# Kernel tuning notes

Measured on AMD Instinct MI355X. Metric: run time of the kernel, lower is better.

## Reference

```python
import jax, jax.numpy as jnp
import numpy as np

B, L, D, H, E, K = 4, 2048, 1024, 2048, 8, 2


def _mlp(x, w1, b1, w2, b2):
    # Mlp: Linear -> GELU(tanh) -> Linear (dropout disabled / eval mode)
    h = jax.nn.gelu(x @ w1 + b1, approximate=True)
    return h @ w2 + b2


def setup_inputs() -> dict:
    key = jax.random.key(0)
    ks = jax.random.split(key, 16)
    s = 0.02
    inp = {
        "x": jax.random.normal(ks[0], (B, L, D), dtype=jnp.float32),
        "task_ids": jax.random.randint(ks[1], (B,), 0, 9),
        # gate: Linear(D,H) -> GELU -> Linear(H,E)  (zero-init in source; randomized here for a meaningful routing test)
        "gw1": jax.random.normal(ks[2], (D, H), dtype=jnp.float32) * s,
        "gb1": jnp.zeros((H,), dtype=jnp.float32),
        "gw2": jax.random.normal(ks[3], (H, E), dtype=jnp.float32) * s,
        "gb2": jnp.zeros((E,), dtype=jnp.float32),
        # routed experts, stacked [E, ...]
        "We1": jax.random.normal(ks[4], (E, D, H), dtype=jnp.float32) * s,
        "be1": jnp.zeros((E, H), dtype=jnp.float32),
        "We2": jax.random.normal(ks[5], (E, H, D), dtype=jnp.float32) * s,
        "be2": jnp.zeros((E, D), dtype=jnp.float32),
        # shared expert
        "Ws1": jax.random.normal(ks[6], (D, H), dtype=jnp.float32) * s,
        "bs1": jnp.zeros((H,), dtype=jnp.float32),
        "Ws2": jax.random.normal(ks[7], (H, D), dtype=jnp.float32) * s,
        "bs2": jnp.zeros((D,), dtype=jnp.float32),
    }
    return inp


def reference(x, task_ids, gw1, gb1, gw2, gb2, We1, be1, We2, be2, Ws1, bs1, Ws2, bs2):
    bsz, length, d = x.shape
    T = bsz * length
    xf = x.reshape(T, d)

    # ---- top-k gating (single gate: moe_multiple_gate=False) ----
    logits = jax.nn.gelu(xf @ gw1 + gb1, approximate=False) @ gw2 + gb2  # [T, E]
    scores = jax.nn.softmax(logits, axis=-1)
    topk_w, topk_idx = jax.lax.top_k(scores, K)  # [T, K]
    # dense gate matrix: scatter top-k weights back (matches compute_gating's gates)
    rows = jnp.arange(T)[:, None]
    gates = jnp.zeros_like(scores).at[rows, topk_idx].set(topk_w)  # [T, E]

    # ---- shared expert (always applied) ----
    out = _mlp(xf, Ws1, bs1, Ws2, bs2)

    # ---- routed experts: dense-equivalent of sort/dispatch/scatter-combine ----
    # y += sum_e gates[:, e] * expert_e(x); loop over small fixed E to bound memory
    for e in range(E):
        out = out + gates[:, e:e + 1] * _mlp(xf, We1[e], be1[e], We2[e], be2[e])

    return out.reshape(bsz, length, d)
```

## Files before the change

### kernel.cpp

```cpp
#include <hip/hip_runtime.h>
#include <hip/hip_bf16.h>


using bf16 = __hip_bfloat16;
typedef __attribute__((ext_vector_type(8))) short short8;
typedef __attribute__((ext_vector_type(4))) float float4v;

#define T_TOK 8192
#define DDIM  1024
#define HDIM  2048
#define NEXP  8

__device__ __forceinline__ float bf2f(short s) {
  unsigned u = ((unsigned)(unsigned short)s) << 16;
  return __builtin_bit_cast(float, u);
}
__device__ __forceinline__ unsigned short f2bf(float f) {
  unsigned u = __builtin_bit_cast(unsigned, f);
  unsigned r = (u + 0x7fffu + ((u >> 16) & 1u)) >> 16;
  return (unsigned short)r;
}
__device__ __forceinline__ float gelu_erf_f(float x) {
  return 0.5f * x * (1.0f + erff(x * 0.70710678118654752f));
}
__device__ __forceinline__ float gelu_tanh_f(float x) {
  float t = tanhf(0.7978845608028654f * (x + 0.044715f * x * x * x));
  return 0.5f * x * (1.0f + t);
}
__device__ __forceinline__ void gld_lds16(const bf16* g, bf16* l) {
  __builtin_amdgcn_global_load_lds(
      (const __attribute__((address_space(1))) void*)g,
      (__attribute__((address_space(3))) void*)l, 16, 0, 0);
}

__global__ __launch_bounds__(256) void cast_split_x(
    const float* __restrict__ x, bf16* __restrict__ xh, bf16* __restrict__ xl)
{
  long i = ((long)blockIdx.x * 256 + threadIdx.x) * 4;
  float4v v = *(const float4v*)(x + i);
  short4 h, l;
  short* hp = (short*)&h; short* lp = (short*)&l;
  #pragma unroll
  for (int j = 0; j < 4; ++j) {
    unsigned short hb = f2bf(v[j]);
    hp[j] = (short)hb;
    lp[j] = (short)f2bf(v[j] - bf2f((short)hb));
  }
  *(short4*)((short*)xh + i) = h;
  *(short4*)((short*)xl + i) = l;
}

template<bool SPLIT>
__global__ __launch_bounds__(256) void transpose_cast(
    const float* __restrict__ in, bf16* __restrict__ out,
    bf16* __restrict__ outl, int R, int C)
{
  __shared__ float tile[32][33];
  long b = blockIdx.z;
  const float* ip = in + b * (long)R * C;
  short* op = (short*)out + b * (long)R * C;
  short* opl = SPLIT ? (short*)outl + b * (long)R * C : nullptr;
  int c0 = blockIdx.x * 32, r0 = blockIdx.y * 32;
  int tx = threadIdx.x & 31, ty = threadIdx.x >> 5;
  #pragma unroll
  for (int i = ty; i < 32; i += 8)
    tile[i][tx] = ip[(long)(r0 + i) * C + c0 + tx];
  __syncthreads();
  #pragma unroll
  for (int i = ty; i < 32; i += 8) {
    float v = tile[tx][i];
    unsigned short hb = f2bf(v);
    op[(long)(c0 + i) * R + r0 + tx] = (short)hb;
    if (SPLIT)
      opl[(long)(c0 + i) * R + r0 + tx] = (short)f2bf(v - bf2f((short)hb));
  }
}

template<int ACT, typename OutT, int GATHER, bool WEIGHTED, bool SPLIT, bool COMBINE>
__global__ __launch_bounds__(256) void gemm_bt(
    const bf16* __restrict__ A, const bf16* __restrict__ Bt,
    const bf16* __restrict__ Al, const bf16* __restrict__ Btl,
    const float* __restrict__ bias, OutT* __restrict__ Cmat,
    int M, int N, int Kd, int ldA,
    long strideB, long strideBias,
    const int* __restrict__ perm, const int* __restrict__ counts,
    const float* __restrict__ wslot, const bf16* __restrict__ RoutC)
{
  __shared__ __align__(16) bf16 lA[128 * 32];
  __shared__ __align__(16) bf16 lB[128 * 32];
  __shared__ int permT[128];

  const int tid = threadIdx.x;
  const int tile_n = blockIdx.x, tile_m = blockIdx.y, z = blockIdx.z;

  int Meff = M;
  if (GATHER) {
    const int* perm_z = perm + (long)z * T_TOK;
    Meff = counts[z];
    if (tile_m * 128 >= Meff) return;
    if (tid < 128) {
      int i = tile_m * 128 + tid;
      permT[tid] = perm_z[i < Meff ? i : (Meff - 1)];
    }
    __syncthreads();
  }
  const float* biasz = bias + (long)z * strideBias;

  const int i0 = tid >> 2;
  const int kc = (((tid & 3) ^ ((tid >> 2) & 3))) * 8;
  long rowA0, rowA1;
  if (GATHER) {
    int p0 = permT[i0], p1 = permT[i0 + 64];
    rowA0 = (GATHER == 1) ? (p0 >> 1) : p0;
    rowA1 = (GATHER == 1) ? (p1 >> 1) : p1;
  } else {
    rowA0 = (long)tile_m * 128 + i0;
    rowA1 = rowA0 + 64;
  }
  bf16* lA0 = &lA[tid * 8];
  bf16* lA1 = &lA[(tid + 256) * 8];
  bf16* lB0 = &lB[tid * 8];
  bf16* lB1 = &lB[(tid + 256) * 8];

  const int lane = tid & 63;
  const int wave = tid >> 6;
  const int wm = (wave & 1) * 64;
  const int wn = (wave >> 1) * 64;
  const int fr = lane & 15;
  const int sw = (((lane >> 4) ^ (lane & 3))) * 8;

  float4v acc[4][4];
  #pragma unroll
  for (int i = 0; i < 4; ++i)
    #pragma unroll
    for (int j = 0; j < 4; ++j) acc[i][j] = {0.f, 0.f, 0.f, 0.f};

  #pragma unroll 1
  for (int ps = 0; ps < (SPLIT ? 3 : 1); ++ps) {
    const bf16* Ap = (SPLIT && ps == 2) ? Al : A;
    const bf16* Bp = (SPLIT && ps == 1) ? Btl : Bt;
    const bf16* aBase0 = Ap + rowA0 * ldA + kc;
    const bf16* aBase1 = Ap + rowA1 * ldA + kc;
    const bf16* bBase0 = Bp + (long)z * strideB
                       + ((long)tile_n * 128 + i0) * Kd + kc;
    const bf16* bBase1 = bBase0 + (long)64 * Kd;

    for (int k0 = 0; k0 < Kd; k0 += 32) {
      gld_lds16(aBase0 + k0, lA0);
      gld_lds16(aBase1 + k0, lA1);
      gld_lds16(bBase0 + k0, lB0);
      gld_lds16(bBase1 + k0, lB1);
      __syncthreads();

      short8 af[4], bfr[4];
      #pragma unroll
      for (int mi = 0; mi < 4; ++mi)
        af[mi] = *(const short8*)&lA[(wm + mi * 16 + fr) * 32 + sw];
      #pragma unroll
      for (int ni = 0; ni < 4; ++ni)
        bfr[ni] = *(const short8*)&lB[(wn + ni * 16 + fr) * 32 + sw];
      #pragma unroll
      for (int mi = 0; mi < 4; ++mi)
        #pragma unroll
        for (int ni = 0; ni < 4; ++ni)
          acc[mi][ni] = __builtin_amdgcn_mfma_f32_16x16x32_bf16(
              af[mi], bfr[ni], acc[mi][ni], 0, 0, 0);
      __syncthreads();
    }
  }

  const int rq = ((lane >> 4)) * 4;
  #pragma unroll
  for (int mi = 0; mi < 4; ++mi) {
    #pragma unroll
    for (int r = 0; r < 4; ++r) {
      int irow = wm + mi * 16 + rq + r;
      int gi = tile_m * 128 + irow;
      long crow;
      bool valid = true;
      float w = 1.f;
      if (GATHER) {
        valid = gi < Meff;
        int p = permT[irow];
        crow = p;
        if (WEIGHTED) w = valid ? wslot[p] : 0.f;
      } else {
        crow = gi;
      }
      if (valid) {
        #pragma unroll
        for (int ni = 0; ni < 4; ++ni) {
          int gcol = tile_n * 128 + wn + ni * 16 + fr;
          float v = acc[mi][ni][r] + biasz[gcol];
          if (ACT == 1) v = gelu_erf_f(v);
          else if (ACT == 2) v = gelu_tanh_f(v);
          if (WEIGHTED) v *= w;
          if (COMBINE) {
            const short* rs = (const short*)RoutC;
            v += bf2f(rs[(2 * crow) * DDIM + gcol])
               + bf2f(rs[(2 * crow + 1) * DDIM + gcol]);
          }
          long cidx = crow * (long)N + gcol;
          if (sizeof(OutT) == 4) ((float*)Cmat)[cidx] = v;
          else ((unsigned short*)Cmat)[cidx] = f2bf(v);
        }
      }
    }
  }
}

__global__ __launch_bounds__(256) void logits_kernel(
    const float* __restrict__ G1, const float* __restrict__ gw2,
    const float* __restrict__ gb2, int* __restrict__ tidx,
    float* __restrict__ wslot)
{
  int wv = threadIdx.x >> 6, lane = threadIdx.x & 63;
  int t = blockIdx.x * 4 + wv;
  const float* grow = G1 + (long)t * HDIM;
  float acc[NEXP];
  #pragma unroll
  for (int e = 0; e < NEXP; ++e) acc[e] = 0.f;
  for (int j = 0; j < HDIM / 64; ++j) {
    int h = j * 64 + lane;
    float g = grow[h];
    float4v w0 = *(const float4v*)&gw2[h * NEXP];
    float4v w1 = *(const float4v*)&gw2[h * NEXP + 4];
    #pragma unroll
    for (int e = 0; e < 4; ++e) {
      acc[e]     += g * w0[e];
      acc[e + 4] += g * w1[e];
    }
  }
  #pragma unroll
  for (int off = 32; off >= 1; off >>= 1)
    #pragma unroll
    for (int e = 0; e < NEXP; ++e) acc[e] += __shfl_xor(acc[e], off);

  if (lane == 0) {
    float lg[NEXP];
    #pragma unroll
    for (int e = 0; e < NEXP; ++e) lg[e] = acc[e] + gb2[e];
    int i1 = 0;
    for (int e = 1; e < NEXP; ++e) if (lg[e] > lg[i1]) i1 = e;
    int i2 = (i1 == 0) ? 1 : 0;
    for (int e = 0; e < NEXP; ++e) {
      if (e == i1) continue;
      if (lg[e] > lg[i2]) i2 = e;
    }
    float m = lg[i1], s = 0.f;
    #pragma unroll
    for (int e = 0; e < NEXP; ++e) s += expf(lg[e] - m);
    float inv = 1.f / s;
    tidx[2 * t]     = i1;
    tidx[2 * t + 1] = i2;
    wslot[2 * t]     = expf(lg[i1] - m) * inv;
    wslot[2 * t + 1] = expf(lg[i2] - m) * inv;
  }
}

__global__ __launch_bounds__(256) void dispatch_kernel(
    const int* __restrict__ tidx, int* __restrict__ counts,
    int* __restrict__ perm)
{
  int t = blockIdx.x * 256 + threadIdx.x;
  int lane = threadIdx.x & 63;
  #pragma unroll
  for (int k = 0; k < 2; ++k) {
    int e = tidx[2 * t + k];
    #pragma unroll
    for (int ex = 0; ex < NEXP; ++ex) {
      unsigned long long m = __ballot(e == ex);
      if (m) {
        int leader = __ffsll((unsigned long long)m) - 1;
        int base = 0;
        if (lane == leader) base = atomicAdd(&counts[ex], __popcll(m));
        base = __shfl(base, leader);
        if (e == ex) {
          int pos = base + __popcll(m & ((1ULL << lane) - 1ULL));
          perm[ex * T_TOK + pos] = 2 * t + k;
        }
      }
    }
  }
}

extern "C" void kernel_launch(void* const* d_in, const int* in_sizes, int n_in,
                              void* d_out, int out_size, void* d_ws, size_t ws_size,
                              hipStream_t stream)
{
  const float* x   = (const float*)d_in[0];
  const float* gw1 = (const float*)d_in[2];
  const float* gb1 = (const float*)d_in[3];
  const float* gw2 = (const float*)d_in[4];
  const float* gb2 = (const float*)d_in[5];
  const float* We1 = (const float*)d_in[6];
  const float* be1 = (const float*)d_in[7];
  const float* We2 = (const float*)d_in[8];
  const float* be2 = (const float*)d_in[9];
  const float* Ws1 = (const float*)d_in[10];
  const float* bs1 = (const float*)d_in[11];
  const float* Ws2 = (const float*)d_in[12];
  const float* bs2 = (const float*)d_in[13];
  float* out = (float*)d_out;

  char* ws = (char*)d_ws;
  bf16*  xb     = (bf16*)(ws + 0);
  bf16*  We1t   = (bf16*)(ws + 16777216);
  bf16*  Rout   = (bf16*)(ws + 16777216);
  bf16*  We2t   = (bf16*)(ws + 50331648);
  bf16*  Ws1t   = (bf16*)(ws + 83886080);
  bf16*  Ws2t   = (bf16*)(ws + 88080384);
  int*   counts = (int*)(ws + 92274688);
  float* wslot  = (float*)(ws + 92275712);
  int*   perm   = (int*)(ws + 92341248);
  bf16*  xl     = (bf16*)(ws + 92603392);
  bf16*  gw1h   = (bf16*)(ws + 109380608);
  bf16*  gw1l   = (bf16*)(ws + 113574912);
  int*   tidx   = (int*)(ws + 113574912);
  float* G1     = (float*)(ws + 117769216);
  bf16*  Hrt    = (bf16*)(ws + 117769216);
  bf16*  S1     = (bf16*)(ws + 117769216);

  hipMemsetAsync(counts, 0, NEXP * sizeof(int), stream);

  dim3 blk(256);
  cast_split_x<<<dim3((T_TOK * DDIM) / 1024), blk, 0, stream>>>(x, xb, xl);
  transpose_cast<true ><<<dim3(HDIM/32, DDIM/32, 1), blk, 0, stream>>>(gw1, gw1h, gw1l, DDIM, HDIM);
  transpose_cast<false><<<dim3(HDIM/32, DDIM/32, 1), blk, 0, stream>>>(Ws1, Ws1t, nullptr, DDIM, HDIM);
  transpose_cast<false><<<dim3(DDIM/32, HDIM/32, 1), blk, 0, stream>>>(Ws2, Ws2t, nullptr, HDIM, DDIM);
  transpose_cast<false><<<dim3(HDIM/32, DDIM/32, NEXP), blk, 0, stream>>>(We1, We1t, nullptr, DDIM, HDIM);
  transpose_cast<false><<<dim3(DDIM/32, HDIM/32, NEXP), blk, 0, stream>>>(We2, We2t, nullptr, HDIM, DDIM);

  gemm_bt<1, float, 0, false, true, false><<<dim3(HDIM/128, T_TOK/128, 1), blk, 0, stream>>>(
      xb, gw1h, xl, gw1l, gb1, G1, T_TOK, HDIM, DDIM, DDIM, 0, 0,
      nullptr, nullptr, nullptr, nullptr);
  logits_kernel<<<dim3(T_TOK / 4), blk, 0, stream>>>(G1, gw2, gb2, tidx, wslot);
  dispatch_kernel<<<dim3(T_TOK / 256), blk, 0, stream>>>(tidx, counts, perm);
  gemm_bt<2, bf16, 1, false, false, false><<<dim3(HDIM/128, T_TOK/128, NEXP), blk, 0, stream>>>(
      xb, We1t, nullptr, nullptr, be1, Hrt, T_TOK, HDIM, DDIM, DDIM,
      (long)HDIM * DDIM, HDIM, perm, counts, nullptr, nullptr);
  gemm_bt<0, bf16, 2, true, false, false><<<dim3(DDIM/128, T_TOK/128, NEXP), blk, 0, stream>>>(
      Hrt, We2t, nullptr, nullptr, be2, Rout, T_TOK, DDIM, HDIM, HDIM,
      (long)DDIM * HDIM, DDIM, perm, counts, wslot, nullptr);
  gemm_bt<2, bf16, 0, false, false, false><<<dim3(HDIM/128, T_TOK/128, 1), blk, 0, stream>>>(
      xb, Ws1t, nullptr, nullptr, bs1, S1, T_TOK, HDIM, DDIM, DDIM, 0, 0,
      nullptr, nullptr, nullptr, nullptr);
  gemm_bt<0, float, 0, false, false, true><<<dim3(DDIM/128, T_TOK/128, 1), blk, 0, stream>>>(
      S1, Ws2t, nullptr, nullptr, bs2, out, T_TOK, DDIM, HDIM, HDIM, 0, 0,
      nullptr, nullptr, nullptr, Rout);
}
```

Baseline: 892.7 us.

## Double K-tile depth and fuse split-precision passes into one K loop

In the non-split path, each K step of the GEMM now loads a 64-wide K slice instead of 32, using a wider XOR swizzle, so each step does twice the MFMA work per pair of barriers. In the split-precision (hi/lo bf16) path, the three separate passes over K are merged into one loop that stages hi and lo tiles of A and B together and issues all three MFMA products per step. The aim is to cut barrier and loop overhead and to avoid reading A and B from global memory three times. In exchange, LDS use doubles, which may reduce occupancy, and register pressure in the fused split path goes up.

```diff
diff --git a/kernel.cpp b/kernel.cpp
--- a/kernel.cpp
+++ b/kernel.cpp
@@ -86,8 +86,8 @@
     const int* __restrict__ perm, const int* __restrict__ counts,
     const float* __restrict__ wslot, const bf16* __restrict__ RoutC)
 {
-  __shared__ __align__(16) bf16 lA[128 * 32];
-  __shared__ __align__(16) bf16 lB[128 * 32];
+  __shared__ __align__(16) bf16 lA[128 * 64];
+  __shared__ __align__(16) bf16 lB[128 * 64];
   __shared__ int permT[128];
 
   const int tid = threadIdx.x;
@@ -106,28 +106,11 @@
   }
   const float* biasz = bias + (long)z * strideBias;
 
-  const int i0 = tid >> 2;
-  const int kc = (((tid & 3) ^ ((tid >> 2) & 3))) * 8;
-  long rowA0, rowA1;
-  if (GATHER) {
-    int p0 = permT[i0], p1 = permT[i0 + 64];
-    rowA0 = (GATHER == 1) ? (p0 >> 1) : p0;
-    rowA1 = (GATHER == 1) ? (p1 >> 1) : p1;
-  } else {
-    rowA0 = (long)tile_m * 128 + i0;
-    rowA1 = rowA0 + 64;
-  }
-  bf16* lA0 = &lA[tid * 8];
-  bf16* lA1 = &lA[(tid + 256) * 8];
-  bf16* lB0 = &lB[tid * 8];
-  bf16* lB1 = &lB[(tid + 256) * 8];
-
   const int lane = tid & 63;
   const int wave = tid >> 6;
   const int wm = (wave & 1) * 64;
   const int wn = (wave >> 1) * 64;
   const int fr = lane & 15;
-  const int sw = (((lane >> 4) ^ (lane & 3))) * 8;
 
   float4v acc[4][4];
   #pragma unroll
@@ -135,36 +118,113 @@
     #pragma unroll
     for (int j = 0; j < 4; ++j) acc[i][j] = {0.f, 0.f, 0.f, 0.f};
 
-  #pragma unroll 1
-  for (int ps = 0; ps < (SPLIT ? 3 : 1); ++ps) {
-    const bf16* Ap = (SPLIT && ps == 2) ? Al : A;
-    const bf16* Bp = (SPLIT && ps == 1) ? Btl : Bt;
-    const bf16* aBase0 = Ap + rowA0 * ldA + kc;
-    const bf16* aBase1 = Ap + rowA1 * ldA + kc;
-    const bf16* bBase0 = Bp + (long)z * strideB
-                       + ((long)tile_n * 128 + i0) * Kd + kc;
-    const bf16* bBase1 = bBase0 + (long)64 * Kd;
+  if constexpr (SPLIT) {
+    const int i0 = tid >> 2;
+    const int cS = (((tid & 3) ^ ((tid >> 2) & 3) ^ ((tid >> 4) & 1))) * 8;
+    const long rA0 = (long)tile_m * 128 + i0;
+    const long rA1 = rA0 + 64;
+    const long rB0 = (long)tile_n * 128 + i0;
+
+    const bf16* pAh0 = A   + rA0 * ldA + cS;
+    const bf16* pAh1 = A   + rA1 * ldA + cS;
+    const bf16* pAl0 = Al  + rA0 * ldA + cS;
+    const bf16* pAl1 = Al  + rA1 * ldA + cS;
+    const bf16* pBh0 = Bt  + rB0 * Kd + cS;
+    const bf16* pBh1 = pBh0 + (long)64 * Kd;
+    const bf16* pBl0 = Btl + rB0 * Kd + cS;
+    const bf16* pBl1 = pBl0 + (long)64 * Kd;
+
+    bf16* dAh0 = &lA[tid * 8];         bf16* dAh1 = &lA[(tid + 256) * 8];
+    bf16* dAl0 = &lA[4096 + tid * 8];  bf16* dAl1 = &lA[4096 + (tid + 256) * 8];
+    bf16* dBh0 = &lB[tid * 8];         bf16* dBh1 = &lB[(tid + 256) * 8];
+    bf16* dBl0 = &lB[4096 + tid * 8];  bf16* dBl1 = &lB[4096 + (tid + 256) * 8];
+
+    const int sw = (((lane >> 4) ^ (lane & 3) ^ ((lane >> 2) & 1))) * 8;
 
     for (int k0 = 0; k0 < Kd; k0 += 32) {
-      gld_lds16(aBase0 + k0, lA0);
-      gld_lds16(aBase1 + k0, lA1);
-      gld_lds16(bBase0 + k0, lB0);
-      gld_lds16(bBase1 + k0, lB1);
+      gld_lds16(pAh0 + k0, dAh0); gld_lds16(pAh1 + k0, dAh1);
+      gld_lds16(pAl0 + k0, dAl0); gld_lds16(pAl1 + k0, dAl1);
+      gld_lds16(pBh0 + k0, dBh0); gld_lds16(pBh1 + k0, dBh1);
+      gld_lds16(pBl0 + k0, dBl0); gld_lds16(pBl1 + k0, dBl1);
       __syncthreads();
 
-      short8 af[4], bfr[4];
-      #pragma unroll
-      for (int mi = 0; mi < 4; ++mi)
-        af[mi] = *(const short8*)&lA[(wm + mi * 16 + fr) * 32 + sw];
-      #pragma unroll
-      for (int ni = 0; ni < 4; ++ni)
-        bfr[ni] = *(const short8*)&lB[(wn + ni * 16 + fr) * 32 + sw];
+      short8 ah[4], alr[4], bh[4], blr[4];
+      #pragma unroll
+      for (int mi = 0; mi < 4; ++mi) {
+        ah[mi]  = *(const short8*)&lA[(wm + mi * 16 + fr) * 32 + sw];
+        alr[mi] = *(const short8*)&lA[4096 + (wm + mi * 16 + fr) * 32 + sw];
+      }
+      #pragma unroll
+      for (int ni = 0; ni < 4; ++ni) {
+        bh[ni]  = *(const short8*)&lB[(wn + ni * 16 + fr) * 32 + sw];
+        blr[ni] = *(const short8*)&lB[4096 + (wn + ni * 16 + fr) * 32 + sw];
+      }
       #pragma unroll
       for (int mi = 0; mi < 4; ++mi)
         #pragma unroll
         for (int ni = 0; ni < 4; ++ni)
           acc[mi][ni] = __builtin_amdgcn_mfma_f32_16x16x32_bf16(
-              af[mi], bfr[ni], acc[mi][ni], 0, 0, 0);
+              ah[mi], bh[ni], acc[mi][ni], 0, 0, 0);
+      #pragma unroll
+      for (int mi = 0; mi < 4; ++mi)
+        #pragma unroll
+        for (int ni = 0; ni < 4; ++ni)
+          acc[mi][ni] = __builtin_amdgcn_mfma_f32_16x16x32_bf16(
+              ah[mi], blr[ni], acc[mi][ni], 0, 0, 0);
+      #pragma unroll
+      for (int mi = 0; mi < 4; ++mi)
+        #pragma unroll
+        for (int ni = 0; ni < 4; ++ni)
+          acc[mi][ni] = __builtin_amdgcn_mfma_f32_16x16x32_bf16(
+              alr[mi], bh[ni], acc[mi][ni], 0, 0, 0);
+      __syncthreads();
+    }
+  } else {
+    const int r0 = tid >> 3;
+    const int cD = (((tid & 7) ^ ((tid >> 3) & 7))) * 8;
+
+    const bf16* pA[4]; const bf16* pB[4]; bf16* dA[4]; bf16* dB[4];
+    #pragma unroll
+    for (int i = 0; i < 4; ++i) {
+      int rt = i * 32 + r0;
+      long ra;
+      if (GATHER) {
+        int p = permT[rt];
+        ra = (GATHER == 1) ? (long)(p >> 1) : (long)p;
+      } else {
+        ra = (long)tile_m * 128 + rt;
+      }
+      pA[i] = A + ra * ldA + cD;
+      pB[i] = Bt + (long)z * strideB + ((long)tile_n * 128 + rt) * Kd + cD;
+      dA[i] = &lA[(i * 256 + tid) * 8];
+      dB[i] = &lB[(i * 256 + tid) * 8];
+    }
+    const int swb = (((lane >> 4) ^ (lane & 7))) * 8;
+
+    for (int k0 = 0; k0 < Kd; k0 += 64) {
+      #pragma unroll
+      for (int i = 0; i < 4; ++i) gld_lds16(pA[i] + k0, dA[i]);
+      #pragma unroll
+      for (int i = 0; i < 4; ++i) gld_lds16(pB[i] + k0, dB[i]);
+      __syncthreads();
+
+      #pragma unroll
+      for (int kh = 0; kh < 2; ++kh) {
+        const int sw = swb ^ (kh * 32);
+        short8 af[4], bfr[4];
+        #pragma unroll
+        for (int mi = 0; mi < 4; ++mi)
+          af[mi] = *(const short8*)&lA[(wm + mi * 16 + fr) * 64 + sw];
+        #pragma unroll
+        for (int ni = 0; ni < 4; ++ni)
+          bfr[ni] = *(const short8*)&lB[(wn + ni * 16 + fr) * 64 + sw];
+        #pragma unroll
+        for (int mi = 0; mi < 4; ++mi)
+          #pragma unroll
+          for (int ni = 0; ni < 4; ++ni)
+            acc[mi][ni] = __builtin_amdgcn_mfma_f32_16x16x32_bf16(
+                af[mi], bfr[ni], acc[mi][ni], 0, 0, 0);
+      }
       __syncthreads();
     }
   }
```

Result: faster. 798.1 us (-10.6%).

## Use 256x256 double-buffered LDS GEMM tiles with 512 threads

Applied to the files above, without the earlier changes.

Replaces the 128x128, 256-thread GEMM with a 256x256-tile kernel run by 512 threads (8 waves, each computing a 128x64 sub-tile). Global-to-LDS loads are double-buffered so the next K-slice is fetched while the current one feeds MFMA, with one barrier per iteration, and s_setprio is raised around the MFMA bursts. The aim is more data reuse per byte loaded and better latency hiding. The split-precision gate GEMM now does its three hi/lo products inside a single K loop instead of three passes. The cost is 128 KB of LDS per block, which limits occupancy to one block per CU, plus coarser padding waste on the gathered per-expert tiles.

```diff
diff --git a/kernel.cpp b/kernel.cpp
--- a/kernel.cpp
+++ b/kernel.cpp
@@ -77,7 +77,7 @@
 }
 
 template<int ACT, typename OutT, int GATHER, bool WEIGHTED, bool SPLIT, bool COMBINE>
-__global__ __launch_bounds__(256) void gemm_bt(
+__global__ __launch_bounds__(512, 2) void gemm256(
     const bf16* __restrict__ A, const bf16* __restrict__ Bt,
     const bf16* __restrict__ Al, const bf16* __restrict__ Btl,
     const float* __restrict__ bias, OutT* __restrict__ Cmat,
@@ -86,9 +86,8 @@
     const int* __restrict__ perm, const int* __restrict__ counts,
     const float* __restrict__ wslot, const bf16* __restrict__ RoutC)
 {
-  __shared__ __align__(16) bf16 lA[128 * 32];
-  __shared__ __align__(16) bf16 lB[128 * 32];
-  __shared__ int permT[128];
+  __shared__ __align__(16) bf16 lds[65536];
+  __shared__ int permT[256];
 
   const int tid = threadIdx.x;
   const int tile_n = blockIdx.x, tile_m = blockIdx.y, z = blockIdx.z;
@@ -97,85 +96,161 @@
   if (GATHER) {
     const int* perm_z = perm + (long)z * T_TOK;
     Meff = counts[z];
-    if (tile_m * 128 >= Meff) return;
-    if (tid < 128) {
-      int i = tile_m * 128 + tid;
+    if (tile_m * 256 >= Meff) return;
+    if (tid < 256) {
+      int i = tile_m * 256 + tid;
       permT[tid] = perm_z[i < Meff ? i : (Meff - 1)];
     }
     __syncthreads();
   }
   const float* biasz = bias + (long)z * strideBias;
-
-  const int i0 = tid >> 2;
-  const int kc = (((tid & 3) ^ ((tid >> 2) & 3))) * 8;
-  long rowA0, rowA1;
-  if (GATHER) {
-    int p0 = permT[i0], p1 = permT[i0 + 64];
-    rowA0 = (GATHER == 1) ? (p0 >> 1) : p0;
-    rowA1 = (GATHER == 1) ? (p1 >> 1) : p1;
-  } else {
-    rowA0 = (long)tile_m * 128 + i0;
-    rowA1 = rowA0 + 64;
-  }
-  bf16* lA0 = &lA[tid * 8];
-  bf16* lA1 = &lA[(tid + 256) * 8];
-  bf16* lB0 = &lB[tid * 8];
-  bf16* lB1 = &lB[(tid + 256) * 8];
 
   const int lane = tid & 63;
   const int wave = tid >> 6;
-  const int wm = (wave & 1) * 64;
-  const int wn = (wave >> 1) * 64;
+  const int wr = wave >> 2;
+  const int wc = wave & 3;
   const int fr = lane & 15;
-  const int sw = (((lane >> 4) ^ (lane & 3))) * 8;
-
-  float4v acc[4][4];
-  #pragma unroll
-  for (int i = 0; i < 4; ++i)
+  const int kq = lane >> 4;
+
+  float4v acc[8][4];
+  #pragma unroll
+  for (int i = 0; i < 8; ++i)
     #pragma unroll
     for (int j = 0; j < 4; ++j) acc[i][j] = {0.f, 0.f, 0.f, 0.f};
 
-  #pragma unroll 1
-  for (int ps = 0; ps < (SPLIT ? 3 : 1); ++ps) {
-    const bf16* Ap = (SPLIT && ps == 2) ? Al : A;
-    const bf16* Bp = (SPLIT && ps == 1) ? Btl : Bt;
-    const bf16* aBase0 = Ap + rowA0 * ldA + kc;
-    const bf16* aBase1 = Ap + rowA1 * ldA + kc;
-    const bf16* bBase0 = Bp + (long)z * strideB
-                       + ((long)tile_n * 128 + i0) * Kd + kc;
-    const bf16* bBase1 = bBase0 + (long)64 * Kd;
-
-    for (int k0 = 0; k0 < Kd; k0 += 32) {
-      gld_lds16(aBase0 + k0, lA0);
-      gld_lds16(aBase1 + k0, lA1);
-      gld_lds16(bBase0 + k0, lB0);
-      gld_lds16(bBase1 + k0, lB1);
-      __syncthreads();
-
-      short8 af[4], bfr[4];
+  const bf16* pG[8];
+  int dL[8];
+  if constexpr (SPLIT) {
+    const int r4 = tid >> 2;
+    const int cS = (((tid & 3) ^ (r4 & 3) ^ ((r4 >> 2) & 1))) * 8;
+    #pragma unroll
+    for (int i = 0; i < 2; ++i) {
+      long ra = (long)tile_m * 256 + i * 128 + r4;
+      long rb = (long)tile_n * 256 + i * 128 + r4;
+      pG[i]     = A   + ra * ldA + cS;  dL[i]     = i * 4096 + tid * 8;
+      pG[2 + i] = Al  + ra * ldA + cS;  dL[2 + i] = 8192  + i * 4096 + tid * 8;
+      pG[4 + i] = Bt  + rb * Kd  + cS;  dL[4 + i] = 16384 + i * 4096 + tid * 8;
+      pG[6 + i] = Btl + rb * Kd  + cS;  dL[6 + i] = 24576 + i * 4096 + tid * 8;
+    }
+  } else {
+    const int r8 = tid >> 3;
+    const int cD = (((tid & 7) ^ (r8 & 7))) * 8;
+    #pragma unroll
+    for (int i = 0; i < 4; ++i) {
+      int rt = i * 64 + r8;
+      long ra;
+      if (GATHER) {
+        int p = permT[rt];
+        ra = (GATHER == 1) ? (long)(p >> 1) : (long)p;
+      } else {
+        ra = (long)tile_m * 256 + rt;
+      }
+      pG[i]     = A + ra * ldA + cD;
+      dL[i]     = i * 4096 + tid * 8;
+      pG[4 + i] = Bt + (long)z * strideB + ((long)tile_n * 256 + rt) * Kd + cD;
+      dL[4 + i] = 16384 + i * 4096 + tid * 8;
+    }
+  }
+
+  const int NT = Kd / (SPLIT ? 32 : 64);
+  auto stage = [&](int t, int bb) {
+    long k0 = (long)t * (SPLIT ? 32 : 64);
+    #pragma unroll
+    for (int i = 0; i < 8; ++i)
+      gld_lds16(pG[i] + k0, &lds[bb * 32768 + dL[i]]);
+  };
+
+  stage(0, 0);
+  __syncthreads();
+  int cur = 0;
+
+  for (int t = 0; t < NT; ++t) {
+    if (t + 1 < NT) stage(t + 1, cur ^ 1);
+    const int bbase = cur * 32768;
+
+    if constexpr (SPLIT) {
+      const int c = kq;
+      short8 bh[4], bl[4];
       #pragma unroll
-      for (int mi = 0; mi < 4; ++mi)
-        af[mi] = *(const short8*)&lA[(wm + mi * 16 + fr) * 32 + sw];
+      for (int ni = 0; ni < 4; ++ni) {
+        int row = wc * 64 + ni * 16 + fr;
+        int sl = ((c ^ (row & 3) ^ ((row >> 2) & 1))) * 8;
+        bh[ni] = *(const short8*)&lds[bbase + 16384 + row * 32 + sl];
+        bl[ni] = *(const short8*)&lds[bbase + 24576 + row * 32 + sl];
+      }
       #pragma unroll
-      for (int ni = 0; ni < 4; ++ni)
-        bfr[ni] = *(const short8*)&lB[(wn + ni * 16 + fr) * 32 + sw];
+      for (int mh = 0; mh < 2; ++mh) {
+        short8 ah[4], alr[4];
+        #pragma unroll
+        for (int i = 0; i < 4; ++i) {
+          int row = wr * 128 + (mh * 4 + i) * 16 + fr;
+          int sl = ((c ^ (row & 3) ^ ((row >> 2) & 1))) * 8;
+          ah[i]  = *(const short8*)&lds[bbase + row * 32 + sl];
+          alr[i] = *(const short8*)&lds[bbase + 8192 + row * 32 + sl];
+        }
+        __builtin_amdgcn_s_setprio(1);
+        #pragma unroll
+        for (int i = 0; i < 4; ++i)
+          #pragma unroll
+          for (int ni = 0; ni < 4; ++ni)
+            acc[mh * 4 + i][ni] = __builtin_amdgcn_mfma_f32_16x16x32_bf16(
+                ah[i], bh[ni], acc[mh * 4 + i][ni], 0, 0, 0);
+        #pragma unroll
+        for (int i = 0; i < 4; ++i)
+          #pragma unroll
+          for (int ni = 0; ni < 4; ++ni)
+            acc[mh * 4 + i][ni] = __builtin_amdgcn_mfma_f32_16x16x32_bf16(
+                ah[i], bl[ni], acc[mh * 4 + i][ni], 0, 0, 0);
+        #pragma unroll
+        for (int i = 0; i < 4; ++i)
+          #pragma unroll
+          for (int ni = 0; ni < 4; ++ni)
+            acc[mh * 4 + i][ni] = __builtin_amdgcn_mfma_f32_16x16x32_bf16(
+                alr[i], bh[ni], acc[mh * 4 + i][ni], 0, 0, 0);
+        __builtin_amdgcn_s_setprio(0);
+      }
+    } else {
       #pragma unroll
-      for (int mi = 0; mi < 4; ++mi)
-        #pragma unroll
-        for (int ni = 0; ni < 4; ++ni)
-          acc[mi][ni] = __builtin_amdgcn_mfma_f32_16x16x32_bf16(
-              af[mi], bfr[ni], acc[mi][ni], 0, 0, 0);
-      __syncthreads();
-    }
-  }
-
-  const int rq = ((lane >> 4)) * 4;
-  #pragma unroll
-  for (int mi = 0; mi < 4; ++mi) {
+      for (int kh = 0; kh < 2; ++kh) {
+        const int c = kh * 4 + kq;
+        short8 bfr[4];
+        #pragma unroll
+        for (int ni = 0; ni < 4; ++ni) {
+          int row = wc * 64 + ni * 16 + fr;
+          bfr[ni] = *(const short8*)&lds[bbase + 16384 + row * 64
+                                         + ((c ^ (row & 7)) * 8)];
+        }
+        #pragma unroll
+        for (int mh = 0; mh < 2; ++mh) {
+          short8 af[4];
+          #pragma unroll
+          for (int i = 0; i < 4; ++i) {
+            int row = wr * 128 + (mh * 4 + i) * 16 + fr;
+            af[i] = *(const short8*)&lds[bbase + row * 64
+                                         + ((c ^ (row & 7)) * 8)];
+          }
+          __builtin_amdgcn_s_setprio(1);
+          #pragma unroll
+          for (int i = 0; i < 4; ++i)
+            #pragma unroll
+            for (int ni = 0; ni < 4; ++ni)
+              acc[mh * 4 + i][ni] = __builtin_amdgcn_mfma_f32_16x16x32_bf16(
+                  af[i], bfr[ni], acc[mh * 4 + i][ni], 0, 0, 0);
+          __builtin_amdgcn_s_setprio(0);
+        }
+      }
+    }
+    __syncthreads();
+    cur ^= 1;
+  }
+
+  const int rq = kq * 4;
+  #pragma unroll
+  for (int mi = 0; mi < 8; ++mi) {
     #pragma unroll
     for (int r = 0; r < 4; ++r) {
-      int irow = wm + mi * 16 + rq + r;
-      int gi = tile_m * 128 + irow;
+      int irow = wr * 128 + mi * 16 + rq + r;
+      int gi = tile_m * 256 + irow;
       long crow;
       bool valid = true;
       float w = 1.f;
@@ -190,7 +265,7 @@
       if (valid) {
         #pragma unroll
         for (int ni = 0; ni < 4; ++ni) {
-          int gcol = tile_n * 128 + wn + ni * 16 + fr;
+          int gcol = tile_n * 256 + wc * 64 + ni * 16 + fr;
           float v = acc[mi][ni][r] + biasz[gcol];
           if (ACT == 1) v = gelu_erf_f(v);
           else if (ACT == 2) v = gelu_tanh_f(v);
@@ -323,7 +398,7 @@
 
   hipMemsetAsync(counts, 0, NEXP * sizeof(int), stream);
 
-  dim3 blk(256);
+  dim3 blk(256), blk2(512);
   cast_split_x<<<dim3((T_TOK * DDIM) / 1024), blk, 0, stream>>>(x, xb, xl);
   transpose_cast<true ><<<dim3(HDIM/32, DDIM/32, 1), blk, 0, stream>>>(gw1, gw1h, gw1l, DDIM, HDIM);
   transpose_cast<false><<<dim3(HDIM/32, DDIM/32, 1), blk, 0, stream>>>(Ws1, Ws1t, nullptr, DDIM, HDIM);
@@ -331,21 +406,21 @@
   transpose_cast<false><<<dim3(HDIM/32, DDIM/32, NEXP), blk, 0, stream>>>(We1, We1t, nullptr, DDIM, HDIM);
   transpose_cast<false><<<dim3(DDIM/32, HDIM/32, NEXP), blk, 0, stream>>>(We2, We2t, nullptr, HDIM, DDIM);
 
-  gemm_bt<1, float, 0, false, true, false><<<dim3(HDIM/128, T_TOK/128, 1), blk, 0, stream>>>(
+  gemm256<1, float, 0, false, true, false><<<dim3(HDIM/256, T_TOK/256, 1), blk2, 0, stream>>>(
       xb, gw1h, xl, gw1l, gb1, G1, T_TOK, HDIM, DDIM, DDIM, 0, 0,
       nullptr, nullptr, nullptr, nullptr);
   logits_kernel<<<dim3(T_TOK / 4), blk, 0, stream>>>(G1, gw2, gb2, tidx, wslot);
   dispatch_kernel<<<dim3(T_TOK / 256), blk, 0, stream>>>(tidx, counts, perm);
-  gemm_bt<2, bf16, 1, false, false, false><<<dim3(HDIM/128, T_TOK/128, NEXP), blk, 0, stream>>>(
+  gemm256<2, bf16, 1, false, false, false><<<dim3(HDIM/256, T_TOK/256, NEXP), blk2, 0, stream>>>(
       xb, We1t, nullptr, nullptr, be1, Hrt, T_TOK, HDIM, DDIM, DDIM,
       (long)HDIM * DDIM, HDIM, perm, counts, nullptr, nullptr);
-  gemm_bt<0, bf16, 2, true, false, false><<<dim3(DDIM/128, T_TOK/128, NEXP), blk, 0, stream>>>(
+  gemm256<0, bf16, 2, true, false, false><<<dim3(DDIM/256, T_TOK/256, NEXP), blk2, 0, stream>>>(
       Hrt, We2t, nullptr, nullptr, be2, Rout, T_TOK, DDIM, HDIM, HDIM,
       (long)DDIM * HDIM, DDIM, perm, counts, wslot, nullptr);
-  gemm_bt<2, bf16, 0, false, false, false><<<dim3(HDIM/128, T_TOK/128, 1), blk, 0, stream>>>(
+  gemm256<2, bf16, 0, false, false, false><<<dim3(HDIM/256, T_TOK/256, 1), blk2, 0, stream>>>(
       xb, Ws1t, nullptr, nullptr, bs1, S1, T_TOK, HDIM, DDIM, DDIM, 0, 0,
       nullptr, nullptr, nullptr, nullptr);
-  gemm_bt<0, float, 0, false, false, true><<<dim3(DDIM/128, T_TOK/128, 1), blk, 0, stream>>>(
+  gemm256<0, float, 0, false, false, true><<<dim3(DDIM/256, T_TOK/256, 1), blk2, 0, stream>>>(
       S1, Ws2t, nullptr, nullptr, bs2, out, T_TOK, DDIM, HDIM, HDIM, 0, 0,
       nullptr, nullptr, nullptr, Rout);
 }
```

Measured after the change: 849.0 us. 1.05x faster.
